# Kernel optimization log

Measured on AMD Instinct MI355X. Metric: run time of the kernel, lower is better.

## Reference

```python
import jax, jax.numpy as jnp
import numpy as np

B, E, S, H = 4, 1024, 1024, 16
HD = E // H  # head_size = 64
MASK_VALUE = -1000000000.0
W_SCALE = 0.05  # keep pre-softmax logits moderate since original softmax is not max-stabilized


def setup_inputs() -> dict:
    key = jax.random.key(0)
    ks = jax.random.split(key, 7)
    queries = jax.random.normal(ks[0], (B, E, S), jnp.float32)
    keys = jax.random.normal(ks[1], (B, E, S), jnp.float32)
    values = jax.random.normal(ks[2], (B, E, S), jnp.float32)
    # causal multiplicative mask, broadcast over batch
    mask = jnp.broadcast_to(jnp.tril(jnp.ones((S, S), jnp.float32)), (B, S, S))
    Wq = jax.random.normal(ks[3], (H, HD, HD), jnp.float32) * W_SCALE
    Wk = jax.random.normal(ks[4], (H, HD, HD), jnp.float32) * W_SCALE
    Wv = jax.random.normal(ks[5], (H, HD, HD), jnp.float32) * W_SCALE
    Wf = jax.random.normal(ks[6], (E, E), jnp.float32) * W_SCALE
    return dict(queries=queries, keys=keys, values=values, mask=mask,
                Wq=Wq, Wk=Wk, Wv=Wv, Wf=Wf)


def reference(queries, keys, values, mask, Wq, Wk, Wv, Wf):
    # channels-first: [B, E, S] -> split embedding axis into heads: [B, H, HD, S]
    qh = queries.reshape(B, H, HD, S)
    kh = keys.reshape(B, H, HD, S)
    vh = values.reshape(B, H, HD, S)
    # per-head linear projections: W[h] @ x_slice, batched over heads
    q = jnp.einsum('hde,bhes->bhds', Wq, qh)
    k = jnp.einsum('hde,bhes->bhds', Wk, kh)
    v = jnp.einsum('hde,bhes->bhds', Wv, vh)
    # pre_softmax = Q^T @ K / sqrt(head_size)  -> [B, H, S, S]
    pre = jnp.einsum('bhds,bhdt->bhst', q, k) / jnp.sqrt(jnp.float32(HD))
    m = mask[:, None, :, :]  # broadcast mask over heads
    pre = pre * m + (m == 0).astype(jnp.float32) * MASK_VALUE
    # Faithful to original: exp / reduce_sum(axis=-1)[..., None, :]
    # i.e. post[b,h,i,j] = exp(pre[b,h,i,j]) / sum_t exp(pre[b,h,j,t])
    e = jnp.exp(pre)
    post = e / jnp.sum(e, axis=3)[:, :, None, :]
    # values @ post^T : out[b,h,d,i] = sum_j v[b,h,d,j] * post[b,h,i,j]
    out_h = jnp.einsum('bhdj,bhij->bhdi', v, post)
    pre_linear = out_h.reshape(B, E, S)  # concat heads along embedding axis
    return jnp.einsum('ef,bfs->bes', Wf, pre_linear)
```

## Files before the change

### kernel.cpp

```cpp
#include <hip/hip_runtime.h>
#include <hip/hip_bf16.h>
#include <stdint.h>

#define NB 4
#define NH 16
#define HDIM 64
#define NS 1024
#define NE 1024

typedef __bf16 bf16x8 __attribute__((ext_vector_type(8)));
typedef __bf16 bf16x2_t __attribute__((ext_vector_type(2)));
typedef float f32x4 __attribute__((ext_vector_type(4)));
typedef unsigned int uint4v __attribute__((ext_vector_type(4)));
typedef unsigned int uint2v __attribute__((ext_vector_type(2)));
typedef unsigned short u16;

#if defined(__has_builtin)
#if __has_builtin(__builtin_amdgcn_global_load_lds)
#define HAVE_GLDS 1
#endif
#endif

__device__ __forceinline__ u16 f2bf(float f) {
  return __builtin_bit_cast(u16, (__bf16)f);
}
__device__ __forceinline__ unsigned pk2(float a, float b) {
  bf16x2_t v; v[0] = (__bf16)a; v[1] = (__bf16)b;
  return __builtin_bit_cast(unsigned, v);
}
__device__ __forceinline__ float fexp2(float x) {
#if defined(__has_builtin)
#if __has_builtin(__builtin_amdgcn_exp2f)
  return __builtin_amdgcn_exp2f(x);
#else
  return __expf(x * 0.69314718056f);
#endif
#else
  return __expf(x * 0.69314718056f);
#endif
}
__device__ __forceinline__ f32x4 mfma16(bf16x8 a, bf16x8 b, f32x4 c) {
  return __builtin_amdgcn_mfma_f32_16x16x32_bf16(a, b, c, 0, 0, 0);
}
__device__ __forceinline__ bf16x8 ld_bf8(const u16* p) {
  return __builtin_bit_cast(bf16x8, *(const uint4v*)p);
}
#ifdef HAVE_GLDS
__device__ __forceinline__ void gld16(const void* g, void* l) {
  __builtin_amdgcn_global_load_lds(
      (__attribute__((address_space(1))) void*)g,
      (__attribute__((address_space(3))) void*)l, 16, 0, 0);
}
#endif

__global__ __launch_bounds__(256) void proj_kernel(
    const float* __restrict__ q_in, const float* __restrict__ k_in,
    const float* __restrict__ v_in, const float* __restrict__ Wq,
    const float* __restrict__ Wk, const float* __restrict__ Wv,
    const float* __restrict__ Wf,
    u16* __restrict__ qT, u16* __restrict__ kT, u16* __restrict__ vv,
    u16* __restrict__ Wf16)
{
  const int which = blockIdx.z;
  const int tid = threadIdx.x;

  if (which == 3) {
    int chunk = blockIdx.y * 4 + blockIdx.x;
    #pragma unroll
    for (int jj = 0; jj < 4; ++jj) {
      int i = chunk * 1024 + tid + 256 * jj;
      float4 f = ((const float4*)Wf)[i];
      uint2v p;
      p[0] = pk2(f.x, f.y);
      p[1] = pk2(f.z, f.w);
      ((uint2v*)Wf16)[i] = p;
    }
    return;
  }

  const int bh = blockIdx.y;
  const int b = bh >> 4, h = bh & 15;
  const int s0 = blockIdx.x * 256;
  const int w = tid >> 6, l = tid & 63, lr = l & 15, lg = l >> 4;

  const float* x = (which == 0) ? q_in : (which == 1) ? k_in : v_in;
  const float* W = ((which == 0) ? Wq : (which == 1) ? Wk : Wv) + h * 4096;
  const float wsc = (which == 0) ? 0.18033688f : 1.0f;

  __shared__ alignas(16) u16 xT[256][72];
  __shared__ alignas(16) u16 Wl[64][72];

  #pragma unroll
  for (int j = 0; j < 4; ++j) {
    int i = tid * 4 + j;
    int d = i >> 4;
    int e0 = (i & 15) * 4;
    float4 f = *(const float4*)(W + d * 64 + e0);
    uint2v p;
    p[0] = pk2(f.x * wsc, f.y * wsc);
    p[1] = pk2(f.z * wsc, f.w * wsc);
    *(uint2v*)&Wl[d][e0] = p;
  }
  {
    const float* xp = x + ((size_t)b * NE + h * 64) * NS + s0 + tid;
    #pragma unroll
    for (int j = 0; j < 8; ++j) {
      uint4v pk;
      #pragma unroll
      for (int q = 0; q < 4; ++q) {
        float f0 = xp[(size_t)(j * 8 + q * 2) * NS];
        float f1 = xp[(size_t)(j * 8 + q * 2 + 1) * NS];
        pk[q] = pk2(f0, f1);
      }
      *(uint4v*)&xT[tid][j * 8] = pk;
    }
  }
  __syncthreads();

  bf16x8 af[4][2];
  #pragma unroll
  for (int mt = 0; mt < 4; ++mt) {
    af[mt][0] = ld_bf8(&Wl[mt * 16 + lr][lg * 8]);
    af[mt][1] = ld_bf8(&Wl[mt * 16 + lr][32 + lg * 8]);
  }
  f32x4 acc[4][4] = {};
  #pragma unroll
  for (int nt = 0; nt < 4; ++nt) {
    bf16x8 b0 = ld_bf8(&xT[w * 64 + nt * 16 + lr][lg * 8]);
    bf16x8 b1 = ld_bf8(&xT[w * 64 + nt * 16 + lr][32 + lg * 8]);
    #pragma unroll
    for (int mt = 0; mt < 4; ++mt) {
      acc[mt][nt] = mfma16(af[mt][0], b0, acc[mt][nt]);
      acc[mt][nt] = mfma16(af[mt][1], b1, acc[mt][nt]);
    }
  }

  if (which < 2) {
    u16* o = ((which == 0) ? qT : kT) + (size_t)bh * NS * 64;
    #pragma unroll
    for (int mt = 0; mt < 4; ++mt)
      #pragma unroll
      for (int nt = 0; nt < 4; ++nt) {
        int s = s0 + w * 64 + nt * 16 + lr;
        int d = mt * 16 + lg * 4;
        uint2v p;
        p[0] = pk2(acc[mt][nt][0], acc[mt][nt][1]);
        p[1] = pk2(acc[mt][nt][2], acc[mt][nt][3]);
        *(uint2v*)(o + (size_t)s * 64 + d) = p;
      }
  } else {
    u16* o = vv + (size_t)bh * 64 * NS;
    #pragma unroll
    for (int mt = 0; mt < 4; ++mt)
      #pragma unroll
      for (int nt = 0; nt < 4; ++nt)
        #pragma unroll
        for (int jr = 0; jr < 4; ++jr) {
          int d = mt * 16 + lg * 4 + jr;
          int s = s0 + w * 64 + nt * 16 + lr;
          o[(size_t)d * NS + s] = f2bf(acc[mt][nt][jr]);
        }
  }
}

__global__ __launch_bounds__(512) void denom_kernel(
    const u16* __restrict__ qT, const u16* __restrict__ kT,
    float* __restrict__ l2rDg)
{
  const int wg = blockIdx.x;
  const int rt = 7 - (wg >> 6);
  const int bh = wg & 63;
  const int i0 = rt * 128;
  const int tid = threadIdx.x, w = tid >> 6, l = tid & 63, lr = l & 15, lg = l >> 4;
  __shared__ alignas(16) u16 klds[128][72];
  const u16* qb = qT + (size_t)bh * NS * 64;
  const u16* kb = kT + (size_t)bh * NS * 64;
  const int gi = i0 + w * 16 + lr;
  bf16x8 bq0 = ld_bf8(qb + (size_t)gi * 64 + lg * 8);
  bf16x8 bq1 = ld_bf8(qb + (size_t)gi * 64 + 32 + lg * 8);
  float den = 0.f;
  const int nkt = rt + 1;
  uint4v kreg[2];
  const int krow = tid >> 3, kcx = tid & 7;
  #pragma unroll
  for (int j = 0; j < 2; ++j)
    kreg[j] = *(const uint4v*)(kb + (size_t)(krow + j * 64) * 64 + kcx * 8);
  for (int t = 0; t < nkt; ++t) {
    __syncthreads();
    #pragma unroll
    for (int j = 0; j < 2; ++j)
      *(uint4v*)&klds[krow + j * 64][kcx * 8] = kreg[j];
    __syncthreads();
    const int t0 = t * 128;
    if (t + 1 < nkt) {
      #pragma unroll
      for (int j = 0; j < 2; ++j)
        kreg[j] = *(const uint4v*)(kb + (size_t)(t0 + 128 + krow + j * 64) * 64 + kcx * 8);
    }
    if (t + 1 < nkt) {
      #pragma unroll
      for (int mt = 0; mt < 8; ++mt) {
        bf16x8 a0 = ld_bf8(&klds[mt * 16 + lr][lg * 8]);
        bf16x8 a1 = ld_bf8(&klds[mt * 16 + lr][32 + lg * 8]);
        f32x4 z = {0.f, 0.f, 0.f, 0.f};
        f32x4 sc = mfma16(a0, bq0, z);
        sc = mfma16(a1, bq1, sc);
        den += fexp2(sc[0]) + fexp2(sc[1]) + fexp2(sc[2]) + fexp2(sc[3]);
      }
    } else {
      #pragma unroll
      for (int mt = 0; mt < 8; ++mt) {
        bf16x8 a0 = ld_bf8(&klds[mt * 16 + lr][lg * 8]);
        bf16x8 a1 = ld_bf8(&klds[mt * 16 + lr][32 + lg * 8]);
        f32x4 z = {0.f, 0.f, 0.f, 0.f};
        f32x4 sc = mfma16(a0, bq0, z);
        sc = mfma16(a1, bq1, sc);
        #pragma unroll
        for (int r = 0; r < 4; ++r) {
          int gt = t0 + mt * 16 + lg * 4 + r;
          den += (gt <= gi) ? fexp2(sc[r]) : 0.f;
        }
      }
    }
  }
  den += __shfl_xor(den, 16);
  den += __shfl_xor(den, 32);
  if (l < 16) l2rDg[(size_t)bh * NS + gi] = -__log2f(den);
}

__global__ __launch_bounds__(256) void attn_kernel(
    const u16* __restrict__ qT, const u16* __restrict__ kT,
    const u16* __restrict__ vv, const float* __restrict__ l2rDg,
    u16* __restrict__ X)
{
  const int wg = blockIdx.x;
  const int rt = 15 - (wg >> 6);
  const int bh = wg & 63;
  const int b = bh >> 4, h = bh & 15;
  const int i0 = rt * 64;
  const int tid = threadIdx.x, w = tid >> 6, l = tid & 63, lr = l & 15, lg = l >> 4;
  __shared__ alignas(16) u16 klds[64][72];
  __shared__ alignas(16) u16 vlds[64][72];
  __shared__ alignas(16) u16 plds[4][16][72];
  __shared__ alignas(16) float dlds[64];
  const u16* qb = qT + (size_t)bh * NS * 64;
  const u16* kb = kT + (size_t)bh * NS * 64;
  const u16* vb = vv + (size_t)bh * 64 * NS;
  const float* rb = l2rDg + (size_t)bh * NS;
  const int gi = i0 + w * 16 + lr;
  bf16x8 bq0 = ld_bf8(qb + (size_t)gi * 64 + lg * 8);
  bf16x8 bq1 = ld_bf8(qb + (size_t)gi * 64 + 32 + lg * 8);
  f32x4 acc[4] = {};
  const int nkt = rt + 1;
  uint4v kreg[2], vreg[2];
  float dreg = 0.f;
  const int krow = tid >> 3, kcx = tid & 7;
  #pragma unroll
  for (int j = 0; j < 2; ++j) {
    kreg[j] = *(const uint4v*)(kb + (size_t)(krow + j * 32) * 64 + kcx * 8);
    vreg[j] = *(const uint4v*)(vb + (size_t)(krow + j * 32) * NS + kcx * 8);
  }
  if (tid < 64) dreg = rb[tid];
  for (int t = 0; t < nkt; ++t) {
    __syncthreads();
    #pragma unroll
    for (int j = 0; j < 2; ++j) {
      *(uint4v*)&klds[krow + j * 32][kcx * 8] = kreg[j];
      *(uint4v*)&vlds[krow + j * 32][kcx * 8] = vreg[j];
    }
    if (tid < 64) dlds[tid] = dreg;
    __syncthreads();
    const int t0 = t * 64;
    if (t + 1 < nkt) {
      const int t0n = t0 + 64;
      #pragma unroll
      for (int j = 0; j < 2; ++j) {
        kreg[j] = *(const uint4v*)(kb + (size_t)(t0n + krow + j * 32) * 64 + kcx * 8);
        vreg[j] = *(const uint4v*)(vb + (size_t)(krow + j * 32) * NS + t0n + kcx * 8);
      }
      if (tid < 64) dreg = rb[t0n + tid];
    }
    const bool diag = (t + 1 == nkt);
    #pragma unroll
    for (int mt = 0; mt < 4; ++mt) {
      if (diag && mt > w) {
        uint2v zz = {0u, 0u};
        *(uint2v*)&plds[w][lr][mt * 16 + lg * 4] = zz;
        continue;
      }
      bf16x8 a0 = ld_bf8(&klds[mt * 16 + lr][lg * 8]);
      bf16x8 a1 = ld_bf8(&klds[mt * 16 + lr][32 + lg * 8]);
      f32x4 z = {0.f, 0.f, 0.f, 0.f};
      f32x4 sc = mfma16(a0, bq0, z);
      sc = mfma16(a1, bq1, sc);
      f32x4 l2 = *(const f32x4*)&dlds[mt * 16 + lg * 4];
      uint2v p;
      if (diag && mt == w) {
        int g0 = t0 + mt * 16 + lg * 4;
        float e0 = (g0 + 0 <= gi) ? fexp2(sc[0] + l2[0]) : 0.f;
        float e1 = (g0 + 1 <= gi) ? fexp2(sc[1] + l2[1]) : 0.f;
        float e2 = (g0 + 2 <= gi) ? fexp2(sc[2] + l2[2]) : 0.f;
        float e3 = (g0 + 3 <= gi) ? fexp2(sc[3] + l2[3]) : 0.f;
        p[0] = pk2(e0, e1);
        p[1] = pk2(e2, e3);
      } else {
        p[0] = pk2(fexp2(sc[0] + l2[0]), fexp2(sc[1] + l2[1]));
        p[1] = pk2(fexp2(sc[2] + l2[2]), fexp2(sc[3] + l2[3]));
      }
      *(uint2v*)&plds[w][lr][mt * 16 + lg * 4] = p;
    }
    bf16x8 ap0 = ld_bf8(&plds[w][lr][lg * 8]);
    bf16x8 ap1 = ld_bf8(&plds[w][lr][32 + lg * 8]);
    __builtin_amdgcn_s_setprio(1);
    #pragma unroll
    for (int nt = 0; nt < 4; ++nt) {
      bf16x8 v0 = ld_bf8(&vlds[nt * 16 + lr][lg * 8]);
      bf16x8 v1 = ld_bf8(&vlds[nt * 16 + lr][32 + lg * 8]);
      acc[nt] = mfma16(ap0, v0, acc[nt]);
      acc[nt] = mfma16(ap1, v1, acc[nt]);
    }
    __builtin_amdgcn_s_setprio(0);
  }
  u16* Xp = X + (size_t)b * NS * NE + h * 64;
  #pragma unroll
  for (int nt = 0; nt < 4; ++nt)
    #pragma unroll
    for (int jr = 0; jr < 4; ++jr) {
      int s = i0 + w * 16 + lg * 4 + jr;
      Xp[(size_t)s * NE + nt * 16 + lr] = f2bf(acc[nt][jr]);
    }
}

__global__ __launch_bounds__(256) void final_gemm(
    const u16* __restrict__ Wf16, const u16* __restrict__ X,
    float* __restrict__ out)
{
  const int b = blockIdx.z;
  const int e0 = blockIdx.y * 128;
  const int s0 = blockIdx.x * 128;
  const int tid = threadIdx.x, w = tid >> 6, l = tid & 63, lr = l & 15, lg = l >> 4;
  const int wm = (w >> 1) * 64, wn = (w & 1) * 64;
  __shared__ alignas(16) u16 Ald[2][128][64];
  __shared__ alignas(16) u16 Bld[2][128][64];
  const u16* Xb = X + (size_t)b * NS * NE;
  f32x4 acc[4][4] = {};

  #define FG_ISSUE(p, k0)                                                     \
    {                                                                         \
      _Pragma("unroll")                                                       \
      for (int j = 0; j < 4; ++j) {                                           \
        int c = tid + 256 * j;                                                \
        int r = c >> 3;                                                       \
        int sc_ = ((c & 7) * 16) ^ ((r & 7) << 4);                            \
        const char* ga = (const char*)(Wf16 + (size_t)(e0 + r) * NE + (k0)) + sc_; \
        const char* gb = (const char*)(Xb + (size_t)(s0 + r) * NE + (k0)) + sc_;   \
        char* la = (char*)&Ald[p][0][0] + c * 16;                             \
        char* lb = (char*)&Bld[p][0][0] + c * 16;                             \
        STAGE16(ga, la);                                                      \
        STAGE16(gb, lb);                                                      \
      }                                                                       \
    }
#ifdef HAVE_GLDS
  #define STAGE16(g, l_) gld16((g), (l_))
#else
  #define STAGE16(g, l_) (*(uint4v*)(l_) = *(const uint4v*)(g))
#endif

  FG_ISSUE(0, 0);
  __syncthreads();
  for (int t = 0; t < 16; ++t) {
    const int p = t & 1;
    if (t < 15) FG_ISSUE(p ^ 1, (t + 1) * 64);
    __builtin_amdgcn_s_setprio(1);
    #pragma unroll
    for (int kk = 0; kk < 2; ++kk) {
      bf16x8 a[4], bb[4];
      #pragma unroll
      for (int mt = 0; mt < 4; ++mt) {
        int R = wm + mt * 16 + lr;
        a[mt] = ld_bf8((const u16*)((const char*)&Ald[p][R][0] +
                                    ((kk * 64 + lg * 16) ^ ((R & 7) << 4))));
      }
      #pragma unroll
      for (int nt = 0; nt < 4; ++nt) {
        int R = wn + nt * 16 + lr;
        bb[nt] = ld_bf8((const u16*)((const char*)&Bld[p][R][0] +
                                     ((kk * 64 + lg * 16) ^ ((R & 7) << 4))));
      }
      #pragma unroll
      for (int mt = 0; mt < 4; ++mt)
        #pragma unroll
        for (int nt = 0; nt < 4; ++nt)
          acc[mt][nt] = mfma16(a[mt], bb[nt], acc[mt][nt]);
    }
    __builtin_amdgcn_s_setprio(0);
    __syncthreads();
  }
  #pragma unroll
  for (int mt = 0; mt < 4; ++mt)
    #pragma unroll
    for (int nt = 0; nt < 4; ++nt) {
      int e = e0 + wm + mt * 16 + lg * 4;
      int s = s0 + wn + nt * 16 + lr;
      float* op = out + ((size_t)b * NE + e) * NS + s;
      op[0] = acc[mt][nt][0];
      op[NS] = acc[mt][nt][1];
      op[2 * NS] = acc[mt][nt][2];
      op[3 * NS] = acc[mt][nt][3];
    }
}

extern "C" void kernel_launch(void* const* d_in, const int* in_sizes, int n_in,
                              void* d_out, int out_size, void* d_ws, size_t ws_size,
                              hipStream_t stream) {
  (void)in_sizes; (void)n_in; (void)out_size; (void)ws_size;
  const float* q_in = (const float*)d_in[0];
  const float* k_in = (const float*)d_in[1];
  const float* v_in = (const float*)d_in[2];
  const float* Wq = (const float*)d_in[4];
  const float* Wk = (const float*)d_in[5];
  const float* Wv = (const float*)d_in[6];
  const float* Wf = (const float*)d_in[7];

  u16* qT = (u16*)d_ws;
  u16* kT = qT + (size_t)NB * NH * NS * HDIM;
  u16* vv = kT + (size_t)NB * NH * NS * HDIM;
  u16* X  = vv + (size_t)NB * NH * HDIM * NS;
  u16* Wf16 = X + (size_t)NB * NS * NE;
  float* l2rD = (float*)(Wf16 + (size_t)NE * NE);

  proj_kernel<<<dim3(4, 64, 4), 256, 0, stream>>>(q_in, k_in, v_in, Wq, Wk, Wv,
                                                  Wf, qT, kT, vv, Wf16);
  denom_kernel<<<dim3(512), 512, 0, stream>>>(qT, kT, l2rD);
  attn_kernel<<<dim3(1024), 256, 0, stream>>>(qT, kT, vv, l2rD, X);
  final_gemm<<<dim3(8, 8, 4), 256, 0, stream>>>(Wf16, X, (float*)d_out);
}
```

Before: 76.38 us.

## Switch denom and attention kernels to 32x32 MFMA with register-resident P

Both the denominator and attention kernels now use 32x32x16 bf16 MFMA tiles, with each wave covering 32 query rows. The attention kernel takes 128-row tiles with half as many blocks. It builds the P operand in registers using permlane32_swap, which drops the LDS round-trip and the zero-fill stores for P. Causal masking skips whole 32-key blocks above the diagonal. The larger accumulator tiles add register pressure, and the smaller grid lowers parallelism.

```diff
diff --git a/kernel.cpp b/kernel.cpp
--- a/kernel.cpp
+++ b/kernel.cpp
@@ -11,6 +11,7 @@
 typedef __bf16 bf16x8 __attribute__((ext_vector_type(8)));
 typedef __bf16 bf16x2_t __attribute__((ext_vector_type(2)));
 typedef float f32x4 __attribute__((ext_vector_type(4)));
+typedef float f32x16 __attribute__((ext_vector_type(16)));
 typedef unsigned int uint4v __attribute__((ext_vector_type(4)));
 typedef unsigned int uint2v __attribute__((ext_vector_type(2)));
 typedef unsigned short u16;
@@ -42,6 +43,9 @@
 __device__ __forceinline__ f32x4 mfma16(bf16x8 a, bf16x8 b, f32x4 c) {
   return __builtin_amdgcn_mfma_f32_16x16x32_bf16(a, b, c, 0, 0, 0);
 }
+__device__ __forceinline__ f32x16 mfma32(bf16x8 a, bf16x8 b, f32x16 c) {
+  return __builtin_amdgcn_mfma_f32_32x32x16_bf16(a, b, c, 0, 0, 0);
+}
 __device__ __forceinline__ bf16x8 ld_bf8(const u16* p) {
   return __builtin_bit_cast(bf16x8, *(const uint4v*)p);
 }
@@ -52,6 +56,25 @@
       (__attribute__((address_space(3))) void*)l, 16, 0, 0);
 }
 #endif
+
+#if defined(__has_builtin)
+#if __has_builtin(__builtin_amdgcn_permlane32_swap)
+#define HAVE_PLS 1
+#endif
+#endif
+__device__ __forceinline__ uint2v plswap(unsigned a, unsigned b) {
+#ifdef HAVE_PLS
+  return __builtin_amdgcn_permlane32_swap(a, b, false, false);
+#else
+  unsigned asw = (unsigned)__shfl_xor((int)a, 32);
+  unsigned bsw = (unsigned)__shfl_xor((int)b, 32);
+  bool hi = (threadIdx.x & 32) != 0;
+  uint2v r;
+  r[0] = hi ? bsw : a;
+  r[1] = hi ? b : asw;
+  return r;
+#endif
+}
 
 __global__ __launch_bounds__(256) void proj_kernel(
     const float* __restrict__ q_in, const float* __restrict__ k_in,
@@ -163,7 +186,7 @@
   }
 }
 
-__global__ __launch_bounds__(512) void denom_kernel(
+__global__ __launch_bounds__(256) void denom_kernel(
     const u16* __restrict__ qT, const u16* __restrict__ kT,
     float* __restrict__ l2rDg)
 {
@@ -171,61 +194,61 @@
   const int rt = 7 - (wg >> 6);
   const int bh = wg & 63;
   const int i0 = rt * 128;
-  const int tid = threadIdx.x, w = tid >> 6, l = tid & 63, lr = l & 15, lg = l >> 4;
+  const int tid = threadIdx.x, w = tid >> 6, l = tid & 63;
+  const int q5 = l & 31, hf = l >> 5;
   __shared__ alignas(16) u16 klds[128][72];
   const u16* qb = qT + (size_t)bh * NS * 64;
   const u16* kb = kT + (size_t)bh * NS * 64;
-  const int gi = i0 + w * 16 + lr;
-  bf16x8 bq0 = ld_bf8(qb + (size_t)gi * 64 + lg * 8);
-  bf16x8 bq1 = ld_bf8(qb + (size_t)gi * 64 + 32 + lg * 8);
+  const int r0w = i0 + w * 32;
+  const int gi2 = r0w + q5;
+  bf16x8 bq[4];
+  #pragma unroll
+  for (int dc = 0; dc < 4; ++dc)
+    bq[dc] = ld_bf8(qb + (size_t)gi2 * 64 + dc * 16 + hf * 8);
   float den = 0.f;
   const int nkt = rt + 1;
-  uint4v kreg[2];
+  uint4v kreg[4];
   const int krow = tid >> 3, kcx = tid & 7;
   #pragma unroll
-  for (int j = 0; j < 2; ++j)
-    kreg[j] = *(const uint4v*)(kb + (size_t)(krow + j * 64) * 64 + kcx * 8);
+  for (int j = 0; j < 4; ++j)
+    kreg[j] = *(const uint4v*)(kb + (size_t)(krow + j * 32) * 64 + kcx * 8);
   for (int t = 0; t < nkt; ++t) {
     __syncthreads();
     #pragma unroll
-    for (int j = 0; j < 2; ++j)
-      *(uint4v*)&klds[krow + j * 64][kcx * 8] = kreg[j];
+    for (int j = 0; j < 4; ++j)
+      *(uint4v*)&klds[krow + j * 32][kcx * 8] = kreg[j];
     __syncthreads();
     const int t0 = t * 128;
     if (t + 1 < nkt) {
       #pragma unroll
-      for (int j = 0; j < 2; ++j)
-        kreg[j] = *(const uint4v*)(kb + (size_t)(t0 + 128 + krow + j * 64) * 64 + kcx * 8);
-    }
-    if (t + 1 < nkt) {
-      #pragma unroll
-      for (int mt = 0; mt < 8; ++mt) {
-        bf16x8 a0 = ld_bf8(&klds[mt * 16 + lr][lg * 8]);
-        bf16x8 a1 = ld_bf8(&klds[mt * 16 + lr][32 + lg * 8]);
-        f32x4 z = {0.f, 0.f, 0.f, 0.f};
-        f32x4 sc = mfma16(a0, bq0, z);
-        sc = mfma16(a1, bq1, sc);
-        den += fexp2(sc[0]) + fexp2(sc[1]) + fexp2(sc[2]) + fexp2(sc[3]);
-      }
-    } else {
-      #pragma unroll
-      for (int mt = 0; mt < 8; ++mt) {
-        bf16x8 a0 = ld_bf8(&klds[mt * 16 + lr][lg * 8]);
-        bf16x8 a1 = ld_bf8(&klds[mt * 16 + lr][32 + lg * 8]);
-        f32x4 z = {0.f, 0.f, 0.f, 0.f};
-        f32x4 sc = mfma16(a0, bq0, z);
-        sc = mfma16(a1, bq1, sc);
-        #pragma unroll
-        for (int r = 0; r < 4; ++r) {
-          int gt = t0 + mt * 16 + lg * 4 + r;
-          den += (gt <= gi) ? fexp2(sc[r]) : 0.f;
+      for (int j = 0; j < 4; ++j)
+        kreg[j] = *(const uint4v*)(kb + (size_t)(t0 + 128 + krow + j * 32) * 64 + kcx * 8);
+    }
+    #pragma unroll
+    for (int kbi = 0; kbi < 4; ++kbi) {
+      const int kb0 = t0 + kbi * 32;
+      if (kb0 > r0w + 31) continue;
+      const bool msk = (kb0 + 31 > r0w);
+      f32x16 sc = {};
+      #pragma unroll
+      for (int dc = 0; dc < 4; ++dc) {
+        bf16x8 ak = ld_bf8(&klds[kbi * 32 + q5][dc * 16 + hf * 8]);
+        sc = mfma32(ak, bq[dc], sc);
+      }
+      if (!msk) {
+        #pragma unroll
+        for (int r = 0; r < 16; ++r) den += fexp2(sc[r]);
+      } else {
+        #pragma unroll
+        for (int r = 0; r < 16; ++r) {
+          int key = kb0 + (r & 3) + 8 * (r >> 2) + 4 * hf;
+          den += (key <= gi2) ? fexp2(sc[r]) : 0.f;
         }
       }
     }
   }
-  den += __shfl_xor(den, 16);
   den += __shfl_xor(den, 32);
-  if (l < 16) l2rDg[(size_t)bh * NS + gi] = -__log2f(den);
+  if (l < 32) l2rDg[(size_t)bh * NS + gi2] = -__log2f(den);
 }
 
 __global__ __launch_bounds__(256) void attn_kernel(
@@ -234,24 +257,27 @@
     u16* __restrict__ X)
 {
   const int wg = blockIdx.x;
-  const int rt = 15 - (wg >> 6);
+  const int rt = 7 - (wg >> 6);
   const int bh = wg & 63;
   const int b = bh >> 4, h = bh & 15;
-  const int i0 = rt * 64;
-  const int tid = threadIdx.x, w = tid >> 6, l = tid & 63, lr = l & 15, lg = l >> 4;
+  const int i0 = rt * 128;
+  const int tid = threadIdx.x, w = tid >> 6, l = tid & 63;
+  const int q5 = l & 31, hf = l >> 5;
   __shared__ alignas(16) u16 klds[64][72];
   __shared__ alignas(16) u16 vlds[64][72];
-  __shared__ alignas(16) u16 plds[4][16][72];
   __shared__ alignas(16) float dlds[64];
   const u16* qb = qT + (size_t)bh * NS * 64;
   const u16* kb = kT + (size_t)bh * NS * 64;
   const u16* vb = vv + (size_t)bh * 64 * NS;
   const float* rb = l2rDg + (size_t)bh * NS;
-  const int gi = i0 + w * 16 + lr;
-  bf16x8 bq0 = ld_bf8(qb + (size_t)gi * 64 + lg * 8);
-  bf16x8 bq1 = ld_bf8(qb + (size_t)gi * 64 + 32 + lg * 8);
-  f32x4 acc[4] = {};
-  const int nkt = rt + 1;
+  const int r0w = i0 + w * 32;
+  const int gi2 = r0w + q5;
+  bf16x8 bq[4];
+  #pragma unroll
+  for (int dc = 0; dc < 4; ++dc)
+    bq[dc] = ld_bf8(qb + (size_t)gi2 * 64 + dc * 16 + hf * 8);
+  f32x16 acc[2] = {};
+  const int nkt = 2 * rt + 2;
   uint4v kreg[2], vreg[2];
   float dreg = 0.f;
   const int krow = tid >> 3, kcx = tid & 7;
@@ -280,54 +306,66 @@
       }
       if (tid < 64) dreg = rb[t0n + tid];
     }
-    const bool diag = (t + 1 == nkt);
-    #pragma unroll
-    for (int mt = 0; mt < 4; ++mt) {
-      if (diag && mt > w) {
-        uint2v zz = {0u, 0u};
-        *(uint2v*)&plds[w][lr][mt * 16 + lg * 4] = zz;
-        continue;
-      }
-      bf16x8 a0 = ld_bf8(&klds[mt * 16 + lr][lg * 8]);
-      bf16x8 a1 = ld_bf8(&klds[mt * 16 + lr][32 + lg * 8]);
-      f32x4 z = {0.f, 0.f, 0.f, 0.f};
-      f32x4 sc = mfma16(a0, bq0, z);
-      sc = mfma16(a1, bq1, sc);
-      f32x4 l2 = *(const f32x4*)&dlds[mt * 16 + lg * 4];
-      uint2v p;
-      if (diag && mt == w) {
-        int g0 = t0 + mt * 16 + lg * 4;
-        float e0 = (g0 + 0 <= gi) ? fexp2(sc[0] + l2[0]) : 0.f;
-        float e1 = (g0 + 1 <= gi) ? fexp2(sc[1] + l2[1]) : 0.f;
-        float e2 = (g0 + 2 <= gi) ? fexp2(sc[2] + l2[2]) : 0.f;
-        float e3 = (g0 + 3 <= gi) ? fexp2(sc[3] + l2[3]) : 0.f;
-        p[0] = pk2(e0, e1);
-        p[1] = pk2(e2, e3);
+    #pragma unroll
+    for (int kbi = 0; kbi < 2; ++kbi) {
+      const int kb0 = t0 + kbi * 32;
+      if (kb0 > r0w + 31) continue;
+      const bool msk = (kb0 + 31 > r0w);
+      f32x16 sc = {};
+      #pragma unroll
+      for (int dc = 0; dc < 4; ++dc) {
+        bf16x8 ak = ld_bf8(&klds[kbi * 32 + q5][dc * 16 + hf * 8]);
+        sc = mfma32(ak, bq[dc], sc);
+      }
+      f32x4 lv[4];
+      #pragma unroll
+      for (int g = 0; g < 4; ++g)
+        lv[g] = *(const f32x4*)&dlds[kbi * 32 + 4 * hf + 8 * g];
+      float p[16];
+      if (!msk) {
+        #pragma unroll
+        for (int r = 0; r < 16; ++r)
+          p[r] = fexp2(sc[r] + lv[r >> 2][r & 3]);
       } else {
-        p[0] = pk2(fexp2(sc[0] + l2[0]), fexp2(sc[1] + l2[1]));
-        p[1] = pk2(fexp2(sc[2] + l2[2]), fexp2(sc[3] + l2[3]));
-      }
-      *(uint2v*)&plds[w][lr][mt * 16 + lg * 4] = p;
-    }
-    bf16x8 ap0 = ld_bf8(&plds[w][lr][lg * 8]);
-    bf16x8 ap1 = ld_bf8(&plds[w][lr][32 + lg * 8]);
-    __builtin_amdgcn_s_setprio(1);
-    #pragma unroll
-    for (int nt = 0; nt < 4; ++nt) {
-      bf16x8 v0 = ld_bf8(&vlds[nt * 16 + lr][lg * 8]);
-      bf16x8 v1 = ld_bf8(&vlds[nt * 16 + lr][32 + lg * 8]);
-      acc[nt] = mfma16(ap0, v0, acc[nt]);
-      acc[nt] = mfma16(ap1, v1, acc[nt]);
-    }
-    __builtin_amdgcn_s_setprio(0);
+        #pragma unroll
+        for (int r = 0; r < 16; ++r) {
+          int key = kb0 + (r & 3) + 8 * (r >> 2) + 4 * hf;
+          float e = fexp2(sc[r] + lv[r >> 2][r & 3]);
+          p[r] = (key <= gi2) ? e : 0.f;
+        }
+      }
+      bf16x8 pa[2];
+      #pragma unroll
+      for (int f = 0; f < 2; ++f) {
+        unsigned A0 = pk2(p[8 * f + 0], p[8 * f + 1]);
+        unsigned A1 = pk2(p[8 * f + 2], p[8 * f + 3]);
+        unsigned B0 = pk2(p[8 * f + 4], p[8 * f + 5]);
+        unsigned B1 = pk2(p[8 * f + 6], p[8 * f + 7]);
+        uint2v s0 = plswap(A0, B0);
+        uint2v s1 = plswap(A1, B1);
+        uint4v fw;
+        fw[0] = s0[0]; fw[1] = s1[0]; fw[2] = s0[1]; fw[3] = s1[1];
+        pa[f] = __builtin_bit_cast(bf16x8, fw);
+      }
+      __builtin_amdgcn_s_setprio(1);
+      #pragma unroll
+      for (int db = 0; db < 2; ++db) {
+        #pragma unroll
+        for (int f = 0; f < 2; ++f) {
+          bf16x8 bv = ld_bf8(&vlds[db * 32 + q5][kbi * 32 + f * 16 + hf * 8]);
+          acc[db] = mfma32(pa[f], bv, acc[db]);
+        }
+      }
+      __builtin_amdgcn_s_setprio(0);
+    }
   }
   u16* Xp = X + (size_t)b * NS * NE + h * 64;
   #pragma unroll
-  for (int nt = 0; nt < 4; ++nt)
-    #pragma unroll
-    for (int jr = 0; jr < 4; ++jr) {
-      int s = i0 + w * 16 + lg * 4 + jr;
-      Xp[(size_t)s * NE + nt * 16 + lr] = f2bf(acc[nt][jr]);
+  for (int db = 0; db < 2; ++db)
+    #pragma unroll
+    for (int r = 0; r < 16; ++r) {
+      int srow = r0w + (r & 3) + 8 * (r >> 2) + 4 * hf;
+      Xp[(size_t)srow * NE + db * 32 + q5] = f2bf(acc[db][r]);
     }
 }
 
@@ -431,7 +469,7 @@
 
   proj_kernel<<<dim3(4, 64, 4), 256, 0, stream>>>(q_in, k_in, v_in, Wq, Wk, Wv,
                                                   Wf, qT, kT, vv, Wf16);
-  denom_kernel<<<dim3(512), 512, 0, stream>>>(qT, kT, l2rD);
-  attn_kernel<<<dim3(1024), 256, 0, stream>>>(qT, kT, vv, l2rD, X);
+  denom_kernel<<<dim3(512), 256, 0, stream>>>(qT, kT, l2rD);
+  attn_kernel<<<dim3(512), 256, 0, stream>>>(qT, kT, vv, l2rD, X);
   final_gemm<<<dim3(8, 8, 4), 256, 0, stream>>>(Wf16, X, (float*)d_out);
 }
```

After: 79.16 us. 1.04x slower.
